# Kernel tuning notes

Measured on AMD Instinct MI355X. Metric: run time of the kernel, lower is better.

The kernel has to match this reference:

```python
import jax, jax.numpy as jnp
import numpy as np
from jax import lax

WIN = 7                      # skimage default win_size
NP_ = WIN * WIN              # pixels per window (2D)
COV_NORM = NP_ / (NP_ - 1)   # sample covariance normalization (use_sample_covariance=True)
K1, K2 = 0.01, 0.03          # skimage defaults


def setup_inputs() -> dict:
    key = jax.random.key(0)
    k1, k2 = jax.random.split(key)
    B, H, W = 64, 512, 512
    predictions = jax.random.uniform(k1, (B, H, W), dtype=jnp.float32)
    labels = jax.random.uniform(k2, (B, H, W), dtype=jnp.float32)
    return {"predictions": predictions, "labels": labels}


def _mean_filter(x):
    # x: [B, 1, H, W] -> valid 7x7 mean filter. Because skimage crops `pad`
    # border pixels before averaging, a VALID convolution reproduces exactly
    # the pixels that survive the crop (reflect padding never enters them).
    kern = jnp.full((1, 1, WIN, WIN), 1.0 / NP_, dtype=x.dtype)
    return lax.conv_general_dilated(x, kern, (1, 1), 'VALID')


def reference(predictions, labels):
    X = predictions[:, None].astype(jnp.float32)  # [B,1,H,W]
    Y = labels[:, None].astype(jnp.float32)

    # per-sample data_range = max(pred,targ) - min(pred,targ)
    dmax = jnp.maximum(X.max(axis=(1, 2, 3)), Y.max(axis=(1, 2, 3)))
    dmin = jnp.minimum(X.min(axis=(1, 2, 3)), Y.min(axis=(1, 2, 3)))
    dr = (dmax - dmin)[:, None, None, None]       # [B,1,1,1]
    C1 = (K1 * dr) ** 2
    C2 = (K2 * dr) ** 2

    ux = _mean_filter(X)
    uy = _mean_filter(Y)
    uxx = _mean_filter(X * X)
    uyy = _mean_filter(Y * Y)
    uxy = _mean_filter(X * Y)

    vx = COV_NORM * (uxx - ux * ux)
    vy = COV_NORM * (uyy - uy * uy)
    vxy = COV_NORM * (uxy - ux * uy)

    S = ((2.0 * ux * uy + C1) * (2.0 * vxy + C2)) / (
        (ux * ux + uy * uy + C1) * (vx + vy + C2))

    mssim = S.mean(axis=(1, 2, 3))  # per-sample SSIM
    return mssim.mean()             # ssim_total / batch_size
```

## Files before the change

kernel.cpp:

```cpp
#include <hip/hip_runtime.h>

#define Hc     512
#define Wc     512
#define OH     506
#define OW     506
#define NPIX   (Hc * Wc)
#define BATCH  64
#define CHUNKS 16

#define BH     14
#define NBAND  37
#define NW     3
#define WPB    4
#define GYD    ((NBAND + WPB - 1) / WPB)
#define NPART  (BATCH * NBAND * NW)

typedef float f32x2 __attribute__((ext_vector_type(2)));
typedef float f32x4 __attribute__((ext_vector_type(4)));

__global__ __launch_bounds__(256) void mm_part_kernel(
    const float* __restrict__ X, const float* __restrict__ Y,
    float* __restrict__ part)
{
    int blk = blockIdx.x;
    int b   = blk >> 4;
    int ch  = blk & 15;
    size_t base = (size_t)b * NPIX + (size_t)ch * (NPIX / CHUNKS);
    const float4* x4 = (const float4*)(X + base);
    const float4* y4 = (const float4*)(Y + base);
    const int n4 = (NPIX / CHUNKS) / 4;

    float mn = 1e38f, mx = -1e38f;
    for (int i = threadIdx.x; i < n4; i += 256) {
        float4 a = x4[i];
        float4 c = y4[i];
        mn = fminf(mn, fminf(fminf(a.x, a.y), fminf(a.z, a.w)));
        mx = fmaxf(mx, fmaxf(fmaxf(a.x, a.y), fmaxf(a.z, a.w)));
        mn = fminf(mn, fminf(fminf(c.x, c.y), fminf(c.z, c.w)));
        mx = fmaxf(mx, fmaxf(fmaxf(c.x, c.y), fmaxf(c.z, c.w)));
    }
    #pragma unroll
    for (int off = 1; off < 64; off <<= 1) {
        mn = fminf(mn, __shfl_xor(mn, off, 64));
        mx = fmaxf(mx, __shfl_xor(mx, off, 64));
    }
    __shared__ float smn[4], smx[4];
    int lane = threadIdx.x & 63, wid = threadIdx.x >> 6;
    if (lane == 0) { smn[wid] = mn; smx[wid] = mx; }
    __syncthreads();
    if (threadIdx.x == 0) {
        mn = fminf(fminf(smn[0], smn[1]), fminf(smn[2], smn[3]));
        mx = fmaxf(fmaxf(smx[0], smx[1]), fmaxf(smx[2], smx[3]));
        part[2 * blk]     = mn;
        part[2 * blk + 1] = mx;
    }
}

__global__ __launch_bounds__(256, 4) void ssim_stream_kernel(
    const float* __restrict__ X, const float* __restrict__ Y,
    const float* __restrict__ mmpart, float* __restrict__ part)
{
    const int lane  = threadIdx.x & 63;
    const int wid   = threadIdx.x >> 6;
    const int chunk = blockIdx.x;
    const int band  = blockIdx.y * WPB + wid;
    const int img   = blockIdx.z;
    if (band >= NBAND) return;

    float mn = 1e38f, mx = -1e38f;
    #pragma unroll
    for (int ch = 0; ch < CHUNKS; ++ch) {
        mn = fminf(mn, mmpart[2 * (img * CHUNKS + ch)]);
        mx = fmaxf(mx, mmpart[2 * (img * CHUNKS + ch) + 1]);
    }
    const float dr = mx - mn;
    const float C1 = (0.01f * dr) * (0.01f * dr);
    const float C2 = (0.03f * dr) * (0.03f * dr);
    const f32x2 C1v = {C1, C1};
    const f32x2 C2v = {C2, C2};
    const f32x2 inv2  = {1.0f / 49.0f, 1.0f / 49.0f};
    const f32x2 covn2 = {49.0f / 48.0f, 49.0f / 48.0f};

    const int cbase  = (chunk == 0) ? 0 : (chunk == 1) ? 248 : 496;
    const int out_lo = (chunk == 0) ? 0 : (chunk == 1) ? 250 : 498;
    const int out_hi = (chunk == 0) ? 249 : (chunk == 1) ? 497 : 505;

    const int col0  = cbase + 4 * lane;
    const int col0c = (col0 < 508) ? col0 : 508;
    f32x2 vm01, vm23;
    {
        float v[4];
        #pragma unroll
        for (int j = 0; j < 4; ++j) {
            int oc = col0 + j;
            v[j] = (oc >= out_lo && oc <= out_hi) ? 1.0f : 0.0f;
        }
        vm01 = (f32x2){v[0], v[1]};
        vm23 = (f32x2){v[2], v[3]};
    }

    const int oy0 = band * BH;
    const int nvalid = (OH - oy0) < BH ? (OH - oy0) : BH;

    const float* px = X + (size_t)img * NPIX + col0c;
    const float* py = Y + (size_t)img * NPIX + col0c;

    f32x2 Vx[2]  = {{0,0},{0,0}}, Vy[2]  = {{0,0},{0,0}};
    f32x2 Vxy[2] = {{0,0},{0,0}}, Vss[2] = {{0,0},{0,0}};

    #define VADD(xa, ya)                                                     \
    {                                                                        \
        f32x2 xl = (xa).lo, xh = (xa).hi, yl = (ya).lo, yh = (ya).hi;        \
        Vx[0] += xl; Vx[1] += xh; Vy[0] += yl; Vy[1] += yh;                  \
        Vxy[0] += xl * yl; Vxy[1] += xh * yh;                                \
        Vss[0] += xl * xl + yl * yl; Vss[1] += xh * xh + yh * yh;            \
    }
    #define VSUB(xa, ya)                                                     \
    {                                                                        \
        f32x2 xl = (xa).lo, xh = (xa).hi, yl = (ya).lo, yh = (ya).hi;        \
        Vx[0] -= xl; Vx[1] -= xh; Vy[0] -= yl; Vy[1] -= yh;                  \
        Vxy[0] -= xl * yl; Vxy[1] -= xh * yh;                                \
        Vss[0] -= xl * xl + yl * yl; Vss[1] -= xh * xh + yh * yh;            \
    }

    #pragma unroll
    for (int k = 0; k < 6; ++k) {
        f32x4 xa = *(const f32x4*)(px + (size_t)(oy0 + k) * Wc);
        f32x4 ya = *(const f32x4*)(py + (size_t)(oy0 + k) * Wc);
        VADD(xa, ya)
    }

    f32x2 acc2 = {0.f, 0.f};

    #define H7(V, W0, W1, W2, W3)                                            \
    {                                                                        \
        float v0 = V[0].x, v1 = V[0].y, v2 = V[1].x, v3 = V[1].y;            \
        float t01 = v0 + v1, u23 = v2 + v3;                                  \
        float P3 = t01 + v2, P4 = t01 + u23;                                 \
        float A3 = __shfl_down(P3, 1, 64);                                   \
        float A4 = __shfl_down(P4, 1, 64);                                   \
        float B1 = __shfl_down(v0, 2, 64);                                   \
        float B2 = __shfl_down(t01, 2, 64);                                  \
        float cc = u23 + A4;                                                 \
        W0 = P4 + A3;                                                        \
        W1 = cc + v1;                                                        \
        W2 = cc + B1;                                                        \
        W3 = (v3 + A4) + B2;                                                 \
    }

    #define SSIM2(wx, wy, wp, ws, vmv)                                       \
    {                                                                        \
        f32x2 ux   = wx * inv2;                                              \
        f32x2 uy   = wy * inv2;                                              \
        f32x2 uxuy = ux * uy;                                                \
        f32x2 u2   = ux * ux + uy * uy;                                      \
        f32x2 vxy  = (wp * inv2 - uxuy) * covn2;                             \
        f32x2 vss  = (ws * inv2 - u2) * covn2;                               \
        f32x2 A1   = uxuy + uxuy + C1v;                                      \
        f32x2 A2   = vxy + vxy + C2v;                                        \
        f32x2 B1   = u2 + C1v;                                               \
        f32x2 B2   = vss + C2v;                                              \
        f32x2 den  = B1 * B2;                                                \
        f32x2 num  = A1 * A2;                                                \
        f32x2 rv   = {__builtin_amdgcn_rcpf(den.x),                          \
                      __builtin_amdgcn_rcpf(den.y)};                         \
        acc2 += num * rv * vmv;                                              \
    }

    #pragma unroll
    for (int g = 0; g < 2; ++g) {
        f32x4 lx[7], ly[7];
        #pragma unroll
        for (int k = 0; k < 7; ++k) {
            int r = oy0 + g * 7 + 6 + k;
            if (r > 511) r = 511;
            lx[k] = *(const f32x4*)(px + (size_t)r * Wc);
            ly[k] = *(const f32x4*)(py + (size_t)r * Wc);
        }
        #pragma unroll
        for (int k = 0; k < 7; ++k) {
            const int tt = g * 7 + k;
            VADD(lx[k], ly[k])
            const float rm = (tt < nvalid) ? 1.0f : 0.0f;
            const f32x2 vmr01 = vm01 * rm;
            const f32x2 vmr23 = vm23 * rm;
            float Wx0, Wx1, Wx2, Wx3;  H7(Vx,  Wx0, Wx1, Wx2, Wx3)
            float Wy0, Wy1, Wy2, Wy3;  H7(Vy,  Wy0, Wy1, Wy2, Wy3)
            float Wp0, Wp1, Wp2, Wp3;  H7(Vxy, Wp0, Wp1, Wp2, Wp3)
            float Ws0, Ws1, Ws2, Ws3;  H7(Vss, Ws0, Ws1, Ws2, Ws3)
            f32x2 wx01 = {Wx0, Wx1}, wx23 = {Wx2, Wx3};
            f32x2 wy01 = {Wy0, Wy1}, wy23 = {Wy2, Wy3};
            f32x2 wp01 = {Wp0, Wp1}, wp23 = {Wp2, Wp3};
            f32x2 ws01 = {Ws0, Ws1}, ws23 = {Ws2, Ws3};
            SSIM2(wx01, wy01, wp01, ws01, vmr01)
            SSIM2(wx23, wy23, wp23, ws23, vmr23)
            int ro = oy0 + tt;
            if (ro > 511) ro = 511;
            f32x4 xo = *(const f32x4*)(px + (size_t)ro * Wc);
            f32x4 yo = *(const f32x4*)(py + (size_t)ro * Wc);
            VSUB(xo, yo)
        }
    }

    #undef SSIM2
    #undef H7
    #undef VADD
    #undef VSUB

    float acc = acc2.x + acc2.y;
    #pragma unroll
    for (int off = 1; off < 64; off <<= 1)
        acc += __shfl_xor(acc, off, 64);
    if (lane == 0)
        part[((size_t)img * NBAND + band) * NW + chunk] = acc;
}

__global__ __launch_bounds__(1024) void final_reduce_kernel(
    const float* __restrict__ part, float* __restrict__ out)
{
    __shared__ double sd[1024];
    double s = 0.0;
    for (int i = threadIdx.x; i < NPART; i += 1024)
        s += (double)part[i];
    sd[threadIdx.x] = s;
    __syncthreads();
    for (int off = 512; off > 0; off >>= 1) {
        if (threadIdx.x < off) sd[threadIdx.x] += sd[threadIdx.x + off];
        __syncthreads();
    }
    if (threadIdx.x == 0)
        out[0] = (float)(sd[0] / ((double)BATCH * OH * OW));
}

extern "C" void kernel_launch(void* const* d_in, const int* in_sizes, int n_in,
                              void* d_out, int out_size, void* d_ws, size_t ws_size,
                              hipStream_t stream) {
    const float* X = (const float*)d_in[0];
    const float* Y = (const float*)d_in[1];
    float* out = (float*)d_out;
    float* ws  = (float*)d_ws;

    float* mmpart = ws;
    float* part   = ws + 2048;

    mm_part_kernel<<<BATCH * CHUNKS, 256, 0, stream>>>(X, Y, mmpart);
    dim3 grid(NW, GYD, BATCH);
    ssim_stream_kernel<<<grid, 64 * WPB, 0, stream>>>(X, Y, mmpart, part);
    final_reduce_kernel<<<1, 1024, 0, stream>>>(part, out);
}
```

Baseline: 84.45 us.

## Use smaller row bands, precompute SSIM constants, stream rows in simple loop

```diff
diff --git a/kernel.cpp b/kernel.cpp
--- a/kernel.cpp
+++ b/kernel.cpp
@@ -8,11 +8,11 @@
 #define BATCH  64
 #define CHUNKS 16
 
-#define BH     14
-#define NBAND  37
+#define BH     8
+#define NBAND  64
 #define NW     3
 #define WPB    4
-#define GYD    ((NBAND + WPB - 1) / WPB)
+#define GYD    (NBAND / WPB)
 #define NPART  (BATCH * NBAND * NW)
 
 typedef float f32x2 __attribute__((ext_vector_type(2)));
@@ -56,26 +56,37 @@
     }
 }
 
-__global__ __launch_bounds__(256, 4) void ssim_stream_kernel(
+__global__ void mm_final_kernel(const float* __restrict__ part,
+                                float* __restrict__ c12)
+{
+    int b = threadIdx.x;
+    if (b < BATCH) {
+        float mn = 1e38f, mx = -1e38f;
+        #pragma unroll
+        for (int ch = 0; ch < CHUNKS; ++ch) {
+            mn = fminf(mn, part[2 * (b * CHUNKS + ch)]);
+            mx = fmaxf(mx, part[2 * (b * CHUNKS + ch) + 1]);
+        }
+        float dr = mx - mn;
+        float c1 = 0.01f * dr;
+        float c2 = 0.03f * dr;
+        c12[2 * b]     = c1 * c1;
+        c12[2 * b + 1] = c2 * c2;
+    }
+}
+
+__global__ __launch_bounds__(256, 8) void ssim_stream_kernel(
     const float* __restrict__ X, const float* __restrict__ Y,
-    const float* __restrict__ mmpart, float* __restrict__ part)
+    const float* __restrict__ c12, float* __restrict__ part)
 {
     const int lane  = threadIdx.x & 63;
     const int wid   = threadIdx.x >> 6;
     const int chunk = blockIdx.x;
     const int band  = blockIdx.y * WPB + wid;
     const int img   = blockIdx.z;
-    if (band >= NBAND) return;
-
-    float mn = 1e38f, mx = -1e38f;
-    #pragma unroll
-    for (int ch = 0; ch < CHUNKS; ++ch) {
-        mn = fminf(mn, mmpart[2 * (img * CHUNKS + ch)]);
-        mx = fmaxf(mx, mmpart[2 * (img * CHUNKS + ch) + 1]);
-    }
-    const float dr = mx - mn;
-    const float C1 = (0.01f * dr) * (0.01f * dr);
-    const float C2 = (0.03f * dr) * (0.03f * dr);
+
+    const float C1 = c12[2 * img];
+    const float C2 = c12[2 * img + 1];
     const f32x2 C1v = {C1, C1};
     const f32x2 C2v = {C2, C2};
     const f32x2 inv2  = {1.0f / 49.0f, 1.0f / 49.0f};
@@ -167,39 +178,29 @@
         acc2 += num * rv * vmv;                                              \
     }
 
-    #pragma unroll
-    for (int g = 0; g < 2; ++g) {
-        f32x4 lx[7], ly[7];
-        #pragma unroll
-        for (int k = 0; k < 7; ++k) {
-            int r = oy0 + g * 7 + 6 + k;
-            if (r > 511) r = 511;
-            lx[k] = *(const f32x4*)(px + (size_t)r * Wc);
-            ly[k] = *(const f32x4*)(py + (size_t)r * Wc);
-        }
-        #pragma unroll
-        for (int k = 0; k < 7; ++k) {
-            const int tt = g * 7 + k;
-            VADD(lx[k], ly[k])
-            const float rm = (tt < nvalid) ? 1.0f : 0.0f;
-            const f32x2 vmr01 = vm01 * rm;
-            const f32x2 vmr23 = vm23 * rm;
-            float Wx0, Wx1, Wx2, Wx3;  H7(Vx,  Wx0, Wx1, Wx2, Wx3)
-            float Wy0, Wy1, Wy2, Wy3;  H7(Vy,  Wy0, Wy1, Wy2, Wy3)
-            float Wp0, Wp1, Wp2, Wp3;  H7(Vxy, Wp0, Wp1, Wp2, Wp3)
-            float Ws0, Ws1, Ws2, Ws3;  H7(Vss, Ws0, Ws1, Ws2, Ws3)
-            f32x2 wx01 = {Wx0, Wx1}, wx23 = {Wx2, Wx3};
-            f32x2 wy01 = {Wy0, Wy1}, wy23 = {Wy2, Wy3};
-            f32x2 wp01 = {Wp0, Wp1}, wp23 = {Wp2, Wp3};
-            f32x2 ws01 = {Ws0, Ws1}, ws23 = {Ws2, Ws3};
-            SSIM2(wx01, wy01, wp01, ws01, vmr01)
-            SSIM2(wx23, wy23, wp23, ws23, vmr23)
-            int ro = oy0 + tt;
-            if (ro > 511) ro = 511;
-            f32x4 xo = *(const f32x4*)(px + (size_t)ro * Wc);
-            f32x4 yo = *(const f32x4*)(py + (size_t)ro * Wc);
-            VSUB(xo, yo)
-        }
+    const float* pxi = px + (size_t)(oy0 + 6) * Wc;
+    const float* pyi = py + (size_t)(oy0 + 6) * Wc;
+    const float* pxo = px + (size_t)oy0 * Wc;
+    const float* pyo = py + (size_t)oy0 * Wc;
+
+    #pragma unroll 2
+    for (int tt = 0; tt < nvalid; ++tt) {
+        f32x4 xi = *(const f32x4*)pxi; pxi += Wc;
+        f32x4 yi = *(const f32x4*)pyi; pyi += Wc;
+        VADD(xi, yi)
+        float Wx0, Wx1, Wx2, Wx3;  H7(Vx,  Wx0, Wx1, Wx2, Wx3)
+        float Wy0, Wy1, Wy2, Wy3;  H7(Vy,  Wy0, Wy1, Wy2, Wy3)
+        float Wp0, Wp1, Wp2, Wp3;  H7(Vxy, Wp0, Wp1, Wp2, Wp3)
+        float Ws0, Ws1, Ws2, Ws3;  H7(Vss, Ws0, Ws1, Ws2, Ws3)
+        f32x2 wx01 = {Wx0, Wx1}, wx23 = {Wx2, Wx3};
+        f32x2 wy01 = {Wy0, Wy1}, wy23 = {Wy2, Wy3};
+        f32x2 wp01 = {Wp0, Wp1}, wp23 = {Wp2, Wp3};
+        f32x2 ws01 = {Ws0, Ws1}, ws23 = {Ws2, Ws3};
+        SSIM2(wx01, wy01, wp01, ws01, vm01)
+        SSIM2(wx23, wy23, wp23, ws23, vm23)
+        f32x4 xo = *(const f32x4*)pxo; pxo += Wc;
+        f32x4 yo = *(const f32x4*)pyo; pyo += Wc;
+        VSUB(xo, yo)
     }
 
     #undef SSIM2
@@ -241,10 +242,12 @@
     float* ws  = (float*)d_ws;
 
     float* mmpart = ws;
-    float* part   = ws + 2048;
+    float* c12    = ws + 2048;
+    float* part   = ws + 2048 + 128;
 
     mm_part_kernel<<<BATCH * CHUNKS, 256, 0, stream>>>(X, Y, mmpart);
+    mm_final_kernel<<<1, 64, 0, stream>>>(mmpart, c12);
     dim3 grid(NW, GYD, BATCH);
-    ssim_stream_kernel<<<grid, 64 * WPB, 0, stream>>>(X, Y, mmpart, part);
+    ssim_stream_kernel<<<grid, 64 * WPB, 0, stream>>>(X, Y, c12, part);
     final_reduce_kernel<<<1, 1024, 0, stream>>>(part, out);
 }
```

New measurement: 89.90 us. 1.06x slower.
